# Optimization experiments

Measured on AMD Instinct MI355X. Metric: run time of the kernel, lower is better.

Reference implementation:

```python
import jax, jax.numpy as jnp
import numpy as np

N = 50000
E = 640000
H = 128


def setup_inputs() -> dict:
    key = jax.random.key(0)
    ks = jax.random.split(key, 16)
    s = 0.02
    return {
        "x": jax.random.uniform(ks[0], (N, 1), dtype=jnp.float32),
        "pre_h": jax.random.normal(ks[1], (N, H), dtype=jnp.float32),
        "edge_index": jax.random.randint(ks[2], (2, E), 0, N, dtype=jnp.int32),
        "edge_attr": jax.random.uniform(ks[3], (E, 1), dtype=jnp.float32),
        # encoder: Linear(1+H, H)
        "W_enc": jax.random.normal(ks[4], (1 + H, H), dtype=jnp.float32) * s,
        "b_enc": jnp.zeros((H,), dtype=jnp.float32),
        # message: Linear(2H+1, H)
        "W_M": jax.random.normal(ks[5], (2 * H + 1, H), dtype=jnp.float32) * s,
        "b_M": jnp.zeros((H,), dtype=jnp.float32),
        # update: Linear(2H, H)
        "W_U": jax.random.normal(ks[6], (2 * H, H), dtype=jnp.float32) * s,
        "b_U": jnp.zeros((H,), dtype=jnp.float32),
        # decoder: Linear(2H, 1)
        "W_dec": jax.random.normal(ks[7], (2 * H, 1), dtype=jnp.float32) * s,
        "b_dec": jnp.zeros((1,), dtype=jnp.float32),
        # terminator: Linear(2H, 1)
        "W_term": jax.random.normal(ks[8], (2 * H, 1), dtype=jnp.float32) * s,
        "b_term": jnp.zeros((1,), dtype=jnp.float32),
    }


def reference(x, pre_h, edge_index, edge_attr,
              W_enc, b_enc, W_M, b_M, W_U, b_U,
              W_dec, b_dec, W_term, b_term):
    n = x.shape[0]
    # Encoder: z = relu(Linear([x, pre_h]))  -> [N, H]
    z = jax.nn.relu(jnp.concatenate([x, pre_h], axis=-1) @ W_enc + b_enc)

    # MPNN processor (PyG flow source_to_target: row=src j, col=dst i)
    src, dst = edge_index[0], edge_index[1]
    z_i = z[dst]  # [E, H]
    z_j = z[src]  # [E, H]
    m = jax.nn.relu(jnp.concatenate([z_i, z_j, edge_attr], axis=-1) @ W_M + b_M)
    agg = jax.ops.segment_max(m, dst, num_segments=n)
    # PyG fills nodes with no incoming edges with 0 for max aggregation;
    # messages are >= 0 (relu) so clamping at 0 matches exactly.
    agg = jnp.maximum(agg, jnp.float32(0.0))
    h = jax.nn.relu(jnp.concatenate([z, agg], axis=-1) @ W_U + b_U)

    # Decoder: y = Linear([z, h]) -> [N, 1]
    y = jnp.concatenate([z, h], axis=-1) @ W_dec + b_dec

    # Terminator
    h_mean = jnp.mean(h, axis=0, keepdims=True)              # [1, H]
    hm = jnp.broadcast_to(h_mean, h.shape)                   # [N, H]
    t = jnp.concatenate([h, hm], axis=-1) @ W_term + b_term  # [N, 1]
    tau = jnp.mean(t, axis=0, keepdims=True)                 # [1, 1]

    return h, y, tau
```

## Files before the change

### kernel.cpp

```cpp
#include <hip/hip_runtime.h>

#define DEVINL __device__ __forceinline__
#define BCAP 64
#define NREP 64

typedef __attribute__((ext_vector_type(8))) short short8;
typedef __attribute__((ext_vector_type(4))) float f32x4;
typedef __attribute__((ext_vector_type(4))) unsigned short ushort4v;
typedef __attribute__((ext_vector_type(8))) unsigned short ushort8v;

DEVINL unsigned short f2bf(float f) {
    unsigned u = __float_as_uint(f);
    u += 0x7fffu + ((u >> 16) & 1u);
    return (unsigned short)(u >> 16);
}
DEVINL float bf2f(unsigned short s) { return __uint_as_float(((unsigned)s) << 16); }

__global__ __launch_bounds__(256) void k_prepw(
    const float* __restrict__ Wenc, const float* __restrict__ WM,
    const float* __restrict__ WU,
    unsigned short* __restrict__ WencT, unsigned short* __restrict__ WM1T,
    unsigned short* __restrict__ WM2T, unsigned short* __restrict__ WUT)
{
    int tid = blockIdx.x * blockDim.x + threadIdx.x;
    int nt = gridDim.x * blockDim.x;
    for (int i = tid; i < 128 * 128; i += nt) {
        int c = i >> 7, k = i & 127;
        WencT[c * 128 + k] = f2bf(Wenc[(1 + k) * 128 + c]);
        WM1T[c * 128 + k]  = f2bf(WM[k * 128 + c]);
        WM2T[c * 128 + k]  = f2bf(WM[(128 + k) * 128 + c]);
    }
    for (int i = tid; i < 128 * 256; i += nt) {
        int c = i >> 8, k = i & 255;
        WUT[c * 256 + k] = f2bf(WU[k * 128 + c]);
    }
}


__global__ __launch_bounds__(256) void k_enc(
    const float* __restrict__ x, const float* __restrict__ preh,
    const unsigned short* __restrict__ WencT, const float* __restrict__ Wenc,
    const float* __restrict__ benc, unsigned short* __restrict__ zc, int N)
{
    int t = threadIdx.x;
    int wave = t >> 6, lane = t & 63;
    int m = lane & 15, quad = lane >> 4;
    int node = blockIdx.x * 16 + m;
    bool valid = node < N;
    int nodec = min(node, N - 1);
    f32x4 acc[2] = {(f32x4)0.f, (f32x4)0.f};
    const float* arow = preh + (size_t)nodec * 128;
#pragma unroll
    for (int kc = 0; kc < 4; ++kc) {
        int k0 = kc * 32 + quad * 8;
        float4 f0 = *(const float4*)(arow + k0);
        float4 f1 = *(const float4*)(arow + k0 + 4);
        short8 bfrag;
        bfrag[0] = (short)f2bf(f0.x); bfrag[1] = (short)f2bf(f0.y);
        bfrag[2] = (short)f2bf(f0.z); bfrag[3] = (short)f2bf(f0.w);
        bfrag[4] = (short)f2bf(f1.x); bfrag[5] = (short)f2bf(f1.y);
        bfrag[6] = (short)f2bf(f1.z); bfrag[7] = (short)f2bf(f1.w);
#pragma unroll
        for (int tt = 0; tt < 2; ++tt) {
            int t8 = wave * 2 + tt;
            short8 afrag = *(const short8*)(WencT + (size_t)(t8 * 16 + m) * 128 + k0);
            acc[tt] = __builtin_amdgcn_mfma_f32_16x16x32_bf16(afrag, bfrag, acc[tt], 0, 0, 0);
        }
    }
    if (!valid) return;
    float xv = x[node];
    unsigned short* orow = zc + (size_t)node * 256;
#pragma unroll
    for (int tt = 0; tt < 2; ++tt) {
        int col = (wave * 2 + tt) * 16 + quad * 4;
        float4 w0v = *(const float4*)(Wenc + col);
        float4 bv  = *(const float4*)(benc + col);
        ushort4v o;
        o[0] = f2bf(fmaxf(acc[tt][0] + xv * w0v.x + bv.x, 0.f));
        o[1] = f2bf(fmaxf(acc[tt][1] + xv * w0v.y + bv.y, 0.f));
        o[2] = f2bf(fmaxf(acc[tt][2] + xv * w0v.z + bv.z, 0.f));
        o[3] = f2bf(fmaxf(acc[tt][3] + xv * w0v.w + bv.w, 0.f));
        *(ushort4v*)(orow + col) = o;
    }
}

__global__ __launch_bounds__(256) void k_pq(
    const unsigned short* __restrict__ zc,
    const unsigned short* __restrict__ WM1T, const unsigned short* __restrict__ WM2T,
    unsigned short* __restrict__ Pb, unsigned short* __restrict__ Qb, int N)
{
    const unsigned short* WT = blockIdx.y ? WM2T : WM1T;
    unsigned short* out = blockIdx.y ? Qb : Pb;
    int t = threadIdx.x;
    int wave = t >> 6, lane = t & 63;
    int m = lane & 15, quad = lane >> 4;
    int node = blockIdx.x * 16 + m;
    bool valid = node < N;
    int nodec = min(node, N - 1);
    f32x4 acc[2] = {(f32x4)0.f, (f32x4)0.f};
    const unsigned short* arow = zc + (size_t)nodec * 256;
#pragma unroll
    for (int kc = 0; kc < 4; ++kc) {
        int k0 = kc * 32 + quad * 8;
        short8 bfrag = *(const short8*)(arow + k0);
#pragma unroll
        for (int tt = 0; tt < 2; ++tt) {
            int t8 = wave * 2 + tt;
            short8 afrag = *(const short8*)(WT + (size_t)(t8 * 16 + m) * 128 + k0);
            acc[tt] = __builtin_amdgcn_mfma_f32_16x16x32_bf16(afrag, bfrag, acc[tt], 0, 0, 0);
        }
    }
    if (!valid) return;
    unsigned short* orow = out + (size_t)node * 128;
#pragma unroll
    for (int tt = 0; tt < 2; ++tt) {
        int col = (wave * 2 + tt) * 16 + quad * 4;
        ushort4v o;
        o[0] = f2bf(acc[tt][0]); o[1] = f2bf(acc[tt][1]);
        o[2] = f2bf(acc[tt][2]); o[3] = f2bf(acc[tt][3]);
        *(ushort4v*)(orow + col) = o;
    }
}

__global__ __launch_bounds__(256) void k_h(
    const unsigned short* __restrict__ zc, const unsigned short* __restrict__ WUT,
    const float* __restrict__ bU, const float* __restrict__ Wd,
    const float* __restrict__ bd, float* __restrict__ h,
    float* __restrict__ y, float* __restrict__ hsumR, int N)
{
    __shared__ float ys[4][16];
    __shared__ float hsb[128];
    int t = threadIdx.x;
    int wave = t >> 6, lane = t & 63;
    int m = lane & 15, quad = lane >> 4;
    int node = blockIdx.x * 16 + m;
    bool valid = node < N;
    int nodec = min(node, N - 1);
    f32x4 acc[2] = {(f32x4)0.f, (f32x4)0.f};
    float py = 0.f;
    const unsigned short* arow = zc + (size_t)nodec * 256;
#pragma unroll
    for (int kc = 0; kc < 8; ++kc) {
        int k0 = kc * 32 + quad * 8;
        short8 bfrag = *(const short8*)(arow + k0);
        if (wave == 0 && kc < 4) {
            float4 wa = *(const float4*)(Wd + k0);
            float4 wb = *(const float4*)(Wd + k0 + 4);
            py += bf2f((unsigned short)bfrag[0]) * wa.x
                + bf2f((unsigned short)bfrag[1]) * wa.y
                + bf2f((unsigned short)bfrag[2]) * wa.z
                + bf2f((unsigned short)bfrag[3]) * wa.w
                + bf2f((unsigned short)bfrag[4]) * wb.x
                + bf2f((unsigned short)bfrag[5]) * wb.y
                + bf2f((unsigned short)bfrag[6]) * wb.z
                + bf2f((unsigned short)bfrag[7]) * wb.w;
        }
#pragma unroll
        for (int tt = 0; tt < 2; ++tt) {
            int t8 = wave * 2 + tt;
            short8 afrag = *(const short8*)(WUT + (size_t)(t8 * 16 + m) * 256 + k0);
            acc[tt] = __builtin_amdgcn_mfma_f32_16x16x32_bf16(afrag, bfrag, acc[tt], 0, 0, 0);
        }
    }
    const float* Wdh = Wd + 128;
    float* orow = h + (size_t)nodec * 128;
#pragma unroll
    for (int tt = 0; tt < 2; ++tt) {
        int col = (wave * 2 + tt) * 16 + quad * 4;
        float4 bv = *(const float4*)(bU + col);
        float4 o;
        o.x = valid ? fmaxf(acc[tt][0] + bv.x, 0.f) : 0.f;
        o.y = valid ? fmaxf(acc[tt][1] + bv.y, 0.f) : 0.f;
        o.z = valid ? fmaxf(acc[tt][2] + bv.z, 0.f) : 0.f;
        o.w = valid ? fmaxf(acc[tt][3] + bv.w, 0.f) : 0.f;
        if (valid) *(float4*)(orow + col) = o;
        float4 wd = *(const float4*)(Wdh + col);
        py += o.x * wd.x + o.y * wd.y + o.z * wd.z + o.w * wd.w;
        float4 s = o;
#pragma unroll
        for (int mask = 1; mask <= 8; mask <<= 1) {
            s.x += __shfl_xor(s.x, mask, 64);
            s.y += __shfl_xor(s.y, mask, 64);
            s.z += __shfl_xor(s.z, mask, 64);
            s.w += __shfl_xor(s.w, mask, 64);
        }
        if (m == 0) *(float4*)&hsb[col] = s;
    }
    py += __shfl_xor(py, 16, 64);
    py += __shfl_xor(py, 32, 64);
    if (lane < 16) ys[wave][lane] = py;
    __syncthreads();
    if (t < 16 && blockIdx.x * 16 + t < N)
        y[blockIdx.x * 16 + t] = ys[0][t] + ys[1][t] + ys[2][t] + ys[3][t] + bd[0];
    if (t < 128)
        atomicAdd(&hsumR[(blockIdx.x & (NREP - 1)) * 128 + t], hsb[t]);
}

__global__ __launch_bounds__(256) void k_scatter(
    const int* __restrict__ ei, const float* __restrict__ attr,
    int* __restrict__ cnt, int2* __restrict__ bucket, int E)
{
    int e = blockIdx.x * blockDim.x + threadIdx.x;
    if (e >= E) return;
    int src = ei[e];
    int dst = ei[E + e];
    float a = attr[e];
    int slot = atomicAdd(&cnt[dst], 1);
    if (slot < BCAP)
        bucket[(size_t)dst * BCAP + slot] = make_int2(src, __float_as_int(a));
}

__global__ __launch_bounds__(256) void k_agg(
    const unsigned short* __restrict__ Pb, const unsigned short* __restrict__ Qb,
    const int2* __restrict__ bucket, const int* __restrict__ cnt,
    const float* __restrict__ w3, const float* __restrict__ bM,
    unsigned short* __restrict__ zc, int N)
{
    int gid = blockIdx.x * blockDim.x + threadIdx.x;
    int i = gid >> 4;
    if (i >= N) return;
    int lane = gid & 15;
    int c0 = lane * 8;
    int deg = min(cnt[i], BCAP);
    const int2* b = bucket + (size_t)i * BCAP;
    float w[8], acc[8];
    {
        float4 wa = *(const float4*)(w3 + c0), wb = *(const float4*)(w3 + c0 + 4);
        w[0] = wa.x; w[1] = wa.y; w[2] = wa.z; w[3] = wa.w;
        w[4] = wb.x; w[5] = wb.y; w[6] = wb.z; w[7] = wb.w;
    }
    const float NI = __uint_as_float(0xff800000u);
#pragma unroll
    for (int u = 0; u < 8; ++u) acc[u] = NI;
    int j = 0;
    for (; j + 3 < deg; j += 4) {
        int2 e0 = b[j], e1 = b[j + 1], e2 = b[j + 2], e3 = b[j + 3];
        short8 q0 = *(const short8*)(Qb + (size_t)e0.x * 128 + c0);
        short8 q1 = *(const short8*)(Qb + (size_t)e1.x * 128 + c0);
        short8 q2 = *(const short8*)(Qb + (size_t)e2.x * 128 + c0);
        short8 q3 = *(const short8*)(Qb + (size_t)e3.x * 128 + c0);
        float a0 = __int_as_float(e0.y), a1 = __int_as_float(e1.y);
        float a2 = __int_as_float(e2.y), a3 = __int_as_float(e3.y);
#pragma unroll
        for (int u = 0; u < 8; ++u) {
            acc[u] = fmaxf(acc[u], fmaf(a0, w[u], bf2f((unsigned short)q0[u])));
            acc[u] = fmaxf(acc[u], fmaf(a1, w[u], bf2f((unsigned short)q1[u])));
            acc[u] = fmaxf(acc[u], fmaf(a2, w[u], bf2f((unsigned short)q2[u])));
            acc[u] = fmaxf(acc[u], fmaf(a3, w[u], bf2f((unsigned short)q3[u])));
        }
    }
    for (; j < deg; ++j) {
        int2 e0 = b[j];
        float a0 = __int_as_float(e0.y);
        short8 q0 = *(const short8*)(Qb + (size_t)e0.x * 128 + c0);
#pragma unroll
        for (int u = 0; u < 8; ++u)
            acc[u] = fmaxf(acc[u], fmaf(a0, w[u], bf2f((unsigned short)q0[u])));
    }
    short8 p = *(const short8*)(Pb + (size_t)i * 128 + c0);
    float4 ba = *(const float4*)(bM + c0), bb = *(const float4*)(bM + c0 + 4);
    float bm[8] = {ba.x, ba.y, ba.z, ba.w, bb.x, bb.y, bb.z, bb.w};
    ushort8v o;
#pragma unroll
    for (int u = 0; u < 8; ++u)
        o[u] = f2bf(fmaxf(bf2f((unsigned short)p[u]) + bm[u] + acc[u], 0.f));
    *(ushort8v*)(zc + (size_t)i * 256 + 128 + c0) = o;
}

__global__ __launch_bounds__(128) void k_tau(
    const float* __restrict__ hsumR, const float* __restrict__ Wt,
    const float* __restrict__ bt, float* __restrict__ tau, int N)
{
    __shared__ float sd[128];
    int t = threadIdx.x;
    float s = 0.f;
#pragma unroll
    for (int r = 0; r < NREP; ++r) s += hsumR[r * 128 + t];
    float v = s * (1.f / (float)N) * (Wt[t] + Wt[128 + t]);
    sd[t] = v;
    __syncthreads();
    for (int o = 64; o > 0; o >>= 1) {
        if (t < o) sd[t] += sd[t + o];
        __syncthreads();
    }
    if (t == 0) tau[0] = sd[0] + bt[0];
}

extern "C" void kernel_launch(void* const* d_in, const int* in_sizes, int n_in,
                              void* d_out, int out_size, void* d_ws, size_t ws_size,
                              hipStream_t stream)
{
    const float* x     = (const float*)d_in[0];
    const float* preh  = (const float*)d_in[1];
    const int*   ei    = (const int*)d_in[2];
    const float* attr  = (const float*)d_in[3];
    const float* Wenc  = (const float*)d_in[4];
    const float* benc  = (const float*)d_in[5];
    const float* WM    = (const float*)d_in[6];
    const float* bM    = (const float*)d_in[7];
    const float* WU    = (const float*)d_in[8];
    const float* bU    = (const float*)d_in[9];
    const float* Wd    = (const float*)d_in[10];
    const float* bd    = (const float*)d_in[11];
    const float* Wterm = (const float*)d_in[12];
    const float* bterm = (const float*)d_in[13];
    int N = in_sizes[0];
    int E = in_sizes[3];

    char* wp = (char*)d_ws;
    unsigned short* zc    = (unsigned short*)wp; wp += (size_t)N * 256 * 2;
    unsigned short* Pb    = (unsigned short*)wp; wp += (size_t)N * 128 * 2;
    unsigned short* Qb    = (unsigned short*)wp; wp += (size_t)N * 128 * 2;
    int2*           bucket= (int2*)wp;           wp += (size_t)N * BCAP * 8;
    int*            cnt   = (int*)wp;            wp += (size_t)N * 4;
    float*          hsumR = (float*)wp;          wp += NREP * 128 * 4;
    unsigned short* WencT = (unsigned short*)wp; wp += 128 * 128 * 2;
    unsigned short* WM1T  = (unsigned short*)wp; wp += 128 * 128 * 2;
    unsigned short* WM2T  = (unsigned short*)wp; wp += 128 * 128 * 2;
    unsigned short* WUT   = (unsigned short*)wp; wp += 128 * 256 * 2;

    float* hout = (float*)d_out;
    float* yout = hout + (size_t)N * 128;
    float* tau  = yout + N;

    int nb16 = (N + 15) / 16;
    hipMemsetAsync(cnt, 0, ((size_t)N + NREP * 128) * sizeof(int), stream);

    k_prepw<<<64, 256, 0, stream>>>(Wenc, WM, WU, WencT, WM1T, WM2T, WUT);
    k_scatter<<<(E + 255) / 256, 256, 0, stream>>>(ei, attr, cnt, bucket, E);
    k_enc<<<nb16, 256, 0, stream>>>(x, preh, WencT, Wenc, benc, zc, N);
    k_pq<<<dim3(nb16, 2), 256, 0, stream>>>(zc, WM1T, WM2T, Pb, Qb, N);
    k_agg<<<(N * 16 + 255) / 256, 256, 0, stream>>>(Pb, Qb, bucket, cnt,
                                                    WM + 256 * 128, bM, zc, N);
    k_h<<<nb16, 256, 0, stream>>>(zc, WUT, bU, Wd, bd, hout, yout, hsumR, N);
    k_tau<<<1, 128, 0, stream>>>(hsumR, Wterm, bterm, tau, N);
}
```

Before: 274.1 us.

## Fuse kernels: merge prep+scatter, encoder+PQ, and aggregation+update

Merges weight preparation and edge bucketing into one launch, fuses the encoder with the P/Q projections by staging z in shared memory, and fuses max-aggregation with the update GEMM by placing the aggregated features in shared memory. This removes several kernel launches and the global round-trips of z into P/Q and of agg into the update step. The concatenated zc buffer shrinks to a z-only buffer. The cost is larger blocks with more register and shared-memory pressure, and aggregation work per block is now coupled with the GEMM, which may lower occupancy or leave load imbalance from varying degree less hidden.

```diff
diff --git a/kernel.cpp b/kernel.cpp
--- a/kernel.cpp
+++ b/kernel.cpp
@@ -16,32 +16,49 @@
 }
 DEVINL float bf2f(unsigned short s) { return __uint_as_float(((unsigned)s) << 16); }
 
-__global__ __launch_bounds__(256) void k_prepw(
+__global__ __launch_bounds__(256) void k_prep(
     const float* __restrict__ Wenc, const float* __restrict__ WM,
     const float* __restrict__ WU,
     unsigned short* __restrict__ WencT, unsigned short* __restrict__ WM1T,
-    unsigned short* __restrict__ WM2T, unsigned short* __restrict__ WUT)
-{
-    int tid = blockIdx.x * blockDim.x + threadIdx.x;
-    int nt = gridDim.x * blockDim.x;
-    for (int i = tid; i < 128 * 128; i += nt) {
-        int c = i >> 7, k = i & 127;
-        WencT[c * 128 + k] = f2bf(Wenc[(1 + k) * 128 + c]);
-        WM1T[c * 128 + k]  = f2bf(WM[k * 128 + c]);
-        WM2T[c * 128 + k]  = f2bf(WM[(128 + k) * 128 + c]);
-    }
-    for (int i = tid; i < 128 * 256; i += nt) {
-        int c = i >> 8, k = i & 255;
-        WUT[c * 256 + k] = f2bf(WU[k * 128 + c]);
-    }
-}
-
-
-__global__ __launch_bounds__(256) void k_enc(
+    unsigned short* __restrict__ WM2T, unsigned short* __restrict__ WUT,
+    const int* __restrict__ ei, const float* __restrict__ attr,
+    int* __restrict__ cnt, int2* __restrict__ bucket, int E)
+{
+    if (blockIdx.x < 64) {
+        int tid = blockIdx.x * 256 + threadIdx.x;
+        const int nt = 64 * 256;
+        for (int i = tid; i < 128 * 128; i += nt) {
+            int c = i >> 7, k = i & 127;
+            WencT[c * 128 + k] = f2bf(Wenc[(1 + k) * 128 + c]);
+            WM1T[c * 128 + k]  = f2bf(WM[k * 128 + c]);
+            WM2T[c * 128 + k]  = f2bf(WM[(128 + k) * 128 + c]);
+        }
+        for (int i = tid; i < 128 * 256; i += nt) {
+            int c = i >> 8, k = i & 255;
+            WUT[c * 256 + k] = f2bf(WU[k * 128 + c]);
+        }
+    } else {
+        int e = (blockIdx.x - 64) * 256 + threadIdx.x;
+        if (e >= E) return;
+        int src = ei[e];
+        int dst = ei[E + e];
+        float a = attr[e];
+        int slot = atomicAdd(&cnt[dst], 1);
+        if (slot < BCAP)
+            bucket[(size_t)dst * BCAP + slot] = make_int2(src, __float_as_int(a));
+    }
+}
+
+
+__global__ __launch_bounds__(256) void k_zpq(
     const float* __restrict__ x, const float* __restrict__ preh,
     const unsigned short* __restrict__ WencT, const float* __restrict__ Wenc,
-    const float* __restrict__ benc, unsigned short* __restrict__ zc, int N)
-{
+    const float* __restrict__ benc,
+    const unsigned short* __restrict__ WM1T, const unsigned short* __restrict__ WM2T,
+    unsigned short* __restrict__ zb, unsigned short* __restrict__ Pb,
+    unsigned short* __restrict__ Qb, int N)
+{
+    __shared__ __align__(16) unsigned short zl[16][136];
     int t = threadIdx.x;
     int wave = t >> 6, lane = t & 63;
     int m = lane & 15, quad = lane >> 4;
@@ -67,9 +84,7 @@
             acc[tt] = __builtin_amdgcn_mfma_f32_16x16x32_bf16(afrag, bfrag, acc[tt], 0, 0, 0);
         }
     }
-    if (!valid) return;
-    float xv = x[node];
-    unsigned short* orow = zc + (size_t)node * 256;
+    float xv = x[nodec];
 #pragma unroll
     for (int tt = 0; tt < 2; ++tt) {
         int col = (wave * 2 + tt) * 16 + quad * 4;
@@ -80,57 +95,105 @@
         o[1] = f2bf(fmaxf(acc[tt][1] + xv * w0v.y + bv.y, 0.f));
         o[2] = f2bf(fmaxf(acc[tt][2] + xv * w0v.z + bv.z, 0.f));
         o[3] = f2bf(fmaxf(acc[tt][3] + xv * w0v.w + bv.w, 0.f));
-        *(ushort4v*)(orow + col) = o;
-    }
-}
-
-__global__ __launch_bounds__(256) void k_pq(
-    const unsigned short* __restrict__ zc,
-    const unsigned short* __restrict__ WM1T, const unsigned short* __restrict__ WM2T,
-    unsigned short* __restrict__ Pb, unsigned short* __restrict__ Qb, int N)
-{
-    const unsigned short* WT = blockIdx.y ? WM2T : WM1T;
-    unsigned short* out = blockIdx.y ? Qb : Pb;
-    int t = threadIdx.x;
-    int wave = t >> 6, lane = t & 63;
-    int m = lane & 15, quad = lane >> 4;
-    int node = blockIdx.x * 16 + m;
-    bool valid = node < N;
-    int nodec = min(node, N - 1);
-    f32x4 acc[2] = {(f32x4)0.f, (f32x4)0.f};
-    const unsigned short* arow = zc + (size_t)nodec * 256;
+        if (valid) *(ushort4v*)(zb + (size_t)node * 128 + col) = o;
+        *(ushort4v*)&zl[m][col] = o;
+    }
+    __syncthreads();
+    f32x4 aP[2] = {(f32x4)0.f, (f32x4)0.f};
+    f32x4 aQ[2] = {(f32x4)0.f, (f32x4)0.f};
 #pragma unroll
     for (int kc = 0; kc < 4; ++kc) {
         int k0 = kc * 32 + quad * 8;
-        short8 bfrag = *(const short8*)(arow + k0);
+        short8 bfrag = *(const short8*)&zl[m][k0];
 #pragma unroll
         for (int tt = 0; tt < 2; ++tt) {
             int t8 = wave * 2 + tt;
-            short8 afrag = *(const short8*)(WT + (size_t)(t8 * 16 + m) * 128 + k0);
-            acc[tt] = __builtin_amdgcn_mfma_f32_16x16x32_bf16(afrag, bfrag, acc[tt], 0, 0, 0);
+            size_t wo = (size_t)(t8 * 16 + m) * 128 + k0;
+            short8 a1 = *(const short8*)(WM1T + wo);
+            aP[tt] = __builtin_amdgcn_mfma_f32_16x16x32_bf16(a1, bfrag, aP[tt], 0, 0, 0);
+            short8 a2 = *(const short8*)(WM2T + wo);
+            aQ[tt] = __builtin_amdgcn_mfma_f32_16x16x32_bf16(a2, bfrag, aQ[tt], 0, 0, 0);
         }
     }
     if (!valid) return;
-    unsigned short* orow = out + (size_t)node * 128;
+    unsigned short* prow = Pb + (size_t)node * 128;
+    unsigned short* qrow = Qb + (size_t)node * 128;
 #pragma unroll
     for (int tt = 0; tt < 2; ++tt) {
         int col = (wave * 2 + tt) * 16 + quad * 4;
-        ushort4v o;
-        o[0] = f2bf(acc[tt][0]); o[1] = f2bf(acc[tt][1]);
-        o[2] = f2bf(acc[tt][2]); o[3] = f2bf(acc[tt][3]);
-        *(ushort4v*)(orow + col) = o;
-    }
-}
-
-__global__ __launch_bounds__(256) void k_h(
-    const unsigned short* __restrict__ zc, const unsigned short* __restrict__ WUT,
+        ushort4v op, oq;
+        op[0] = f2bf(aP[tt][0]); op[1] = f2bf(aP[tt][1]);
+        op[2] = f2bf(aP[tt][2]); op[3] = f2bf(aP[tt][3]);
+        oq[0] = f2bf(aQ[tt][0]); oq[1] = f2bf(aQ[tt][1]);
+        oq[2] = f2bf(aQ[tt][2]); oq[3] = f2bf(aQ[tt][3]);
+        *(ushort4v*)(prow + col) = op;
+        *(ushort4v*)(qrow + col) = oq;
+    }
+}
+
+__global__ __launch_bounds__(256) void k_aggh(
+    const unsigned short* __restrict__ zb, const unsigned short* __restrict__ Pb,
+    const unsigned short* __restrict__ Qb, const int2* __restrict__ bucket,
+    const int* __restrict__ cnt, const float* __restrict__ w3,
+    const float* __restrict__ bM, const unsigned short* __restrict__ WUT,
     const float* __restrict__ bU, const float* __restrict__ Wd,
     const float* __restrict__ bd, float* __restrict__ h,
     float* __restrict__ y, float* __restrict__ hsumR, int N)
 {
+    __shared__ __align__(16) unsigned short al[16][136];
     __shared__ float ys[4][16];
     __shared__ float hsb[128];
     int t = threadIdx.x;
+    {
+        int il = t >> 4, lane16 = t & 15, c0 = lane16 * 8;
+        int i = blockIdx.x * 16 + il;
+        int ic = min(i, N - 1);
+        int deg = min(cnt[ic], BCAP);
+        const int2* b = bucket + (size_t)ic * BCAP;
+        float w[8], acc[8];
+        {
+            float4 wa = *(const float4*)(w3 + c0), wb = *(const float4*)(w3 + c0 + 4);
+            w[0] = wa.x; w[1] = wa.y; w[2] = wa.z; w[3] = wa.w;
+            w[4] = wb.x; w[5] = wb.y; w[6] = wb.z; w[7] = wb.w;
+        }
+        const float NI = __uint_as_float(0xff800000u);
+#pragma unroll
+        for (int u = 0; u < 8; ++u) acc[u] = NI;
+        int j = 0;
+        for (; j + 3 < deg; j += 4) {
+            int2 e0 = b[j], e1 = b[j + 1], e2 = b[j + 2], e3 = b[j + 3];
+            short8 q0 = *(const short8*)(Qb + (size_t)e0.x * 128 + c0);
+            short8 q1 = *(const short8*)(Qb + (size_t)e1.x * 128 + c0);
+            short8 q2 = *(const short8*)(Qb + (size_t)e2.x * 128 + c0);
+            short8 q3 = *(const short8*)(Qb + (size_t)e3.x * 128 + c0);
+            float a0 = __int_as_float(e0.y), a1 = __int_as_float(e1.y);
+            float a2 = __int_as_float(e2.y), a3 = __int_as_float(e3.y);
+#pragma unroll
+            for (int u = 0; u < 8; ++u) {
+                acc[u] = fmaxf(acc[u], fmaf(a0, w[u], bf2f((unsigned short)q0[u])));
+                acc[u] = fmaxf(acc[u], fmaf(a1, w[u], bf2f((unsigned short)q1[u])));
+                acc[u] = fmaxf(acc[u], fmaf(a2, w[u], bf2f((unsigned short)q2[u])));
+                acc[u] = fmaxf(acc[u], fmaf(a3, w[u], bf2f((unsigned short)q3[u])));
+            }
+        }
+        for (; j < deg; ++j) {
+            int2 e0 = b[j];
+            float a0 = __int_as_float(e0.y);
+            short8 q0 = *(const short8*)(Qb + (size_t)e0.x * 128 + c0);
+#pragma unroll
+            for (int u = 0; u < 8; ++u)
+                acc[u] = fmaxf(acc[u], fmaf(a0, w[u], bf2f((unsigned short)q0[u])));
+        }
+        short8 p = *(const short8*)(Pb + (size_t)ic * 128 + c0);
+        float4 ba = *(const float4*)(bM + c0), bb = *(const float4*)(bM + c0 + 4);
+        float bm[8] = {ba.x, ba.y, ba.z, ba.w, bb.x, bb.y, bb.z, bb.w};
+        ushort8v o;
+#pragma unroll
+        for (int u = 0; u < 8; ++u)
+            o[u] = f2bf(fmaxf(bf2f((unsigned short)p[u]) + bm[u] + acc[u], 0.f));
+        *(ushort8v*)&al[il][c0] = o;
+    }
+    __syncthreads();
     int wave = t >> 6, lane = t & 63;
     int m = lane & 15, quad = lane >> 4;
     int node = blockIdx.x * 16 + m;
@@ -138,22 +201,27 @@
     int nodec = min(node, N - 1);
     f32x4 acc[2] = {(f32x4)0.f, (f32x4)0.f};
     float py = 0.f;
-    const unsigned short* arow = zc + (size_t)nodec * 256;
+    const unsigned short* arow = zb + (size_t)nodec * 128;
 #pragma unroll
     for (int kc = 0; kc < 8; ++kc) {
         int k0 = kc * 32 + quad * 8;
-        short8 bfrag = *(const short8*)(arow + k0);
-        if (wave == 0 && kc < 4) {
-            float4 wa = *(const float4*)(Wd + k0);
-            float4 wb = *(const float4*)(Wd + k0 + 4);
-            py += bf2f((unsigned short)bfrag[0]) * wa.x
-                + bf2f((unsigned short)bfrag[1]) * wa.y
-                + bf2f((unsigned short)bfrag[2]) * wa.z
-                + bf2f((unsigned short)bfrag[3]) * wa.w
-                + bf2f((unsigned short)bfrag[4]) * wb.x
-                + bf2f((unsigned short)bfrag[5]) * wb.y
-                + bf2f((unsigned short)bfrag[6]) * wb.z
-                + bf2f((unsigned short)bfrag[7]) * wb.w;
+        short8 bfrag;
+        if (kc < 4) {
+            bfrag = *(const short8*)(arow + k0);
+            if (wave == 0) {
+                float4 wa = *(const float4*)(Wd + k0);
+                float4 wb = *(const float4*)(Wd + k0 + 4);
+                py += bf2f((unsigned short)bfrag[0]) * wa.x
+                    + bf2f((unsigned short)bfrag[1]) * wa.y
+                    + bf2f((unsigned short)bfrag[2]) * wa.z
+                    + bf2f((unsigned short)bfrag[3]) * wa.w
+                    + bf2f((unsigned short)bfrag[4]) * wb.x
+                    + bf2f((unsigned short)bfrag[5]) * wb.y
+                    + bf2f((unsigned short)bfrag[6]) * wb.z
+                    + bf2f((unsigned short)bfrag[7]) * wb.w;
+            }
+        } else {
+            bfrag = *(const short8*)&al[m][(kc - 4) * 32 + quad * 8];
         }
 #pragma unroll
         for (int tt = 0; tt < 2; ++tt) {
@@ -194,77 +262,6 @@
         y[blockIdx.x * 16 + t] = ys[0][t] + ys[1][t] + ys[2][t] + ys[3][t] + bd[0];
     if (t < 128)
         atomicAdd(&hsumR[(blockIdx.x & (NREP - 1)) * 128 + t], hsb[t]);
-}
-
-__global__ __launch_bounds__(256) void k_scatter(
-    const int* __restrict__ ei, const float* __restrict__ attr,
-    int* __restrict__ cnt, int2* __restrict__ bucket, int E)
-{
-    int e = blockIdx.x * blockDim.x + threadIdx.x;
-    if (e >= E) return;
-    int src = ei[e];
-    int dst = ei[E + e];
-    float a = attr[e];
-    int slot = atomicAdd(&cnt[dst], 1);
-    if (slot < BCAP)
-        bucket[(size_t)dst * BCAP + slot] = make_int2(src, __float_as_int(a));
-}
-
-__global__ __launch_bounds__(256) void k_agg(
-    const unsigned short* __restrict__ Pb, const unsigned short* __restrict__ Qb,
-    const int2* __restrict__ bucket, const int* __restrict__ cnt,
-    const float* __restrict__ w3, const float* __restrict__ bM,
-    unsigned short* __restrict__ zc, int N)
-{
-    int gid = blockIdx.x * blockDim.x + threadIdx.x;
-    int i = gid >> 4;
-    if (i >= N) return;
-    int lane = gid & 15;
-    int c0 = lane * 8;
-    int deg = min(cnt[i], BCAP);
-    const int2* b = bucket + (size_t)i * BCAP;
-    float w[8], acc[8];
-    {
-        float4 wa = *(const float4*)(w3 + c0), wb = *(const float4*)(w3 + c0 + 4);
-        w[0] = wa.x; w[1] = wa.y; w[2] = wa.z; w[3] = wa.w;
-        w[4] = wb.x; w[5] = wb.y; w[6] = wb.z; w[7] = wb.w;
-    }
-    const float NI = __uint_as_float(0xff800000u);
-#pragma unroll
-    for (int u = 0; u < 8; ++u) acc[u] = NI;
-    int j = 0;
-    for (; j + 3 < deg; j += 4) {
-        int2 e0 = b[j], e1 = b[j + 1], e2 = b[j + 2], e3 = b[j + 3];
-        short8 q0 = *(const short8*)(Qb + (size_t)e0.x * 128 + c0);
-        short8 q1 = *(const short8*)(Qb + (size_t)e1.x * 128 + c0);
-        short8 q2 = *(const short8*)(Qb + (size_t)e2.x * 128 + c0);
-        short8 q3 = *(const short8*)(Qb + (size_t)e3.x * 128 + c0);
-        float a0 = __int_as_float(e0.y), a1 = __int_as_float(e1.y);
-        float a2 = __int_as_float(e2.y), a3 = __int_as_float(e3.y);
-#pragma unroll
-        for (int u = 0; u < 8; ++u) {
-            acc[u] = fmaxf(acc[u], fmaf(a0, w[u], bf2f((unsigned short)q0[u])));
-            acc[u] = fmaxf(acc[u], fmaf(a1, w[u], bf2f((unsigned short)q1[u])));
-            acc[u] = fmaxf(acc[u], fmaf(a2, w[u], bf2f((unsigned short)q2[u])));
-            acc[u] = fmaxf(acc[u], fmaf(a3, w[u], bf2f((unsigned short)q3[u])));
-        }
-    }
-    for (; j < deg; ++j) {
-        int2 e0 = b[j];
-        float a0 = __int_as_float(e0.y);
-        short8 q0 = *(const short8*)(Qb + (size_t)e0.x * 128 + c0);
-#pragma unroll
-        for (int u = 0; u < 8; ++u)
-            acc[u] = fmaxf(acc[u], fmaf(a0, w[u], bf2f((unsigned short)q0[u])));
-    }
-    short8 p = *(const short8*)(Pb + (size_t)i * 128 + c0);
-    float4 ba = *(const float4*)(bM + c0), bb = *(const float4*)(bM + c0 + 4);
-    float bm[8] = {ba.x, ba.y, ba.z, ba.w, bb.x, bb.y, bb.z, bb.w};
-    ushort8v o;
-#pragma unroll
-    for (int u = 0; u < 8; ++u)
-        o[u] = f2bf(fmaxf(bf2f((unsigned short)p[u]) + bm[u] + acc[u], 0.f));
-    *(ushort8v*)(zc + (size_t)i * 256 + 128 + c0) = o;
 }
 
 __global__ __launch_bounds__(128) void k_tau(
@@ -308,7 +305,7 @@
     int E = in_sizes[3];
 
     char* wp = (char*)d_ws;
-    unsigned short* zc    = (unsigned short*)wp; wp += (size_t)N * 256 * 2;
+    unsigned short* zb    = (unsigned short*)wp; wp += (size_t)N * 128 * 2;
     unsigned short* Pb    = (unsigned short*)wp; wp += (size_t)N * 128 * 2;
     unsigned short* Qb    = (unsigned short*)wp; wp += (size_t)N * 128 * 2;
     int2*           bucket= (int2*)wp;           wp += (size_t)N * BCAP * 8;
@@ -326,12 +323,12 @@
     int nb16 = (N + 15) / 16;
     hipMemsetAsync(cnt, 0, ((size_t)N + NREP * 128) * sizeof(int), stream);
 
-    k_prepw<<<64, 256, 0, stream>>>(Wenc, WM, WU, WencT, WM1T, WM2T, WUT);
-    k_scatter<<<(E + 255) / 256, 256, 0, stream>>>(ei, attr, cnt, bucket, E);
-    k_enc<<<nb16, 256, 0, stream>>>(x, preh, WencT, Wenc, benc, zc, N);
-    k_pq<<<dim3(nb16, 2), 256, 0, stream>>>(zc, WM1T, WM2T, Pb, Qb, N);
-    k_agg<<<(N * 16 + 255) / 256, 256, 0, stream>>>(Pb, Qb, bucket, cnt,
-                                                    WM + 256 * 128, bM, zc, N);
-    k_h<<<nb16, 256, 0, stream>>>(zc, WUT, bU, Wd, bd, hout, yout, hsumR, N);
+    int sb = (E + 255) / 256;
+    k_prep<<<64 + sb, 256, 0, stream>>>(Wenc, WM, WU, WencT, WM1T, WM2T, WUT,
+                                        ei, attr, cnt, bucket, E);
+    k_zpq<<<nb16, 256, 0, stream>>>(x, preh, WencT, Wenc, benc, WM1T, WM2T,
+                                    zb, Pb, Qb, N);
+    k_aggh<<<nb16, 256, 0, stream>>>(zb, Pb, Qb, bucket, cnt, WM + 256 * 128,
+                                     bM, WUT, bU, Wd, bd, hout, yout, hsumR, N);
     k_tau<<<1, 128, 0, stream>>>(hsumR, Wterm, bterm, tau, N);
 }
```

Result: faster. 252.2 us (-8.0%).
